# Kernel tuning notes

Hardware: AMD Instinct MI355X
Metric: run time of the kernel (lower is better)

Reference implementation:

```python
import jax, jax.numpy as jnp
import numpy as np

SOS = 4998
EOS = 4999
SCALING = 2.0


def setup_inputs() -> dict:
    key = jax.random.key(0)
    ks = jax.random.split(key, 12)
    B, T, E, D, A, C, F, ODIM, L = 32, 1000, 512, 1024, 512, 10, 100, 5000, 100
    s = 0.02
    return {
        "hpad": jax.random.normal(ks[0], (B, T, E), jnp.float32),
        "ys": jax.random.randint(ks[1], (B, L), 0, SOS, jnp.int32),
        # AttLoc params
        "w_enc": jax.random.normal(ks[2], (A, E), jnp.float32) * s,
        "b_enc": jnp.zeros((A,), jnp.float32),
        "w_dec": jax.random.normal(ks[3], (A, D), jnp.float32) * s,
        "w_att": jax.random.normal(ks[4], (A, C), jnp.float32) * s,
        "w_conv": jax.random.normal(ks[5], (C, 1, 2 * F + 1), jnp.float32) * s,  # OIH 1D conv kernel
        "w_gvec": jax.random.normal(ks[6], (1, A), jnp.float32) * s,
        "b_gvec": jnp.zeros((1,), jnp.float32),
        # Decoder params
        "embed": jax.random.normal(ks[7], (ODIM, D), jnp.float32) * s,
        "w_ih": jax.random.normal(ks[8], (4 * D, D + E), jnp.float32) * s,
        "w_hh": jax.random.normal(ks[9], (4 * D, D), jnp.float32) * s,
        "b_ih": jnp.zeros((4 * D,), jnp.float32),
        "b_hh": jnp.zeros((4 * D,), jnp.float32),
        "w_out": jax.random.normal(ks[10], (ODIM, D), jnp.float32) * s,
        "b_out": jnp.zeros((ODIM,), jnp.float32),
    }


def _decode(hpad, ys, w_enc, b_enc, w_dec, w_att, w_conv, w_gvec, b_gvec,
            embed, w_ih, w_hh, b_ih, b_hh, w_out, b_out):
    B, T, E = hpad.shape
    D = w_hh.shape[1]
    F = (w_conv.shape[-1] - 1) // 2
    # ys_in = [sos; y] per utterance (all same length -> already padded)
    ys_in = jnp.concatenate([jnp.full((B, 1), SOS, ys.dtype), ys], axis=1)  # [B, olen]
    eys = embed[ys_in]                                                      # [B, olen, D]
    # pre_compute_enc_h = mlp_enc(enc_h)
    pre = jnp.einsum('bte,ae->bta', hpad, w_enc) + b_enc                    # [B, T, A]
    att0 = jnp.full((B, T), 1.0 / T, hpad.dtype)   # uniform init attention (all hlen == T)
    z0 = jnp.zeros((B, D), hpad.dtype)
    c0 = jnp.zeros((B, D), hpad.dtype)

    def step(carry, ey_i):
        z, c, aw = carry
        # location-aware conv over previous attention weights: [B,1,T] -> [B,C,T]
        conv = jax.lax.conv_general_dilated(aw[:, None, :], w_conv, (1,), [(F, F)],
                                            dimension_numbers=('NCH', 'OIH', 'NCH'))
        att_feat = jnp.einsum('bct,ac->bta', conv, w_att)                   # mlp_att
        dec = (z @ w_dec.T)[:, None, :]                                     # mlp_dec, tiled
        e = jnp.tanh(att_feat + pre + dec) @ w_gvec[0] + b_gvec[0]          # [B, T]
        w = jax.nn.softmax(SCALING * e, axis=1)
        ctx = jnp.einsum('bt,bte->be', w, hpad)                             # [B, E]
        # LSTMCell
        x = jnp.concatenate([ey_i, ctx], axis=1)                            # [B, D+E]
        gates = x @ w_ih.T + b_ih + z @ w_hh.T + b_hh
        i_g, f_g, g_g, o_g = jnp.split(gates, 4, axis=1)
        c_new = jax.nn.sigmoid(f_g) * c + jax.nn.sigmoid(i_g) * jnp.tanh(g_g)
        z_new = jax.nn.sigmoid(o_g) * jnp.tanh(c_new)
        return (z_new, c_new, w), z_new

    _, z_all = jax.lax.scan(step, (z0, c0, att0), jnp.swapaxes(eys, 0, 1))  # [olen, B, D]
    y_all = jnp.einsum('obd,vd->obv', z_all, w_out) + b_out                 # [olen, B, odim]
    return jnp.swapaxes(y_all, 0, 1)                                        # [B, olen, odim]


def reference(hpad, ys, w_enc, b_enc, w_dec, w_att, w_conv, w_gvec, b_gvec,
              embed, w_ih, w_hh, b_ih, b_hh, w_out, b_out):
    return _decode(hpad, ys, w_enc, b_enc, w_dec, w_att, w_conv, w_gvec, b_gvec,
                   embed, w_ih, w_hh, b_ih, b_hh, w_out, b_out)
```

## Files before the change

kernel.cpp:

```cpp
#include <hip/hip_runtime.h>
#include <math.h>

#define B_    32
#define T_    1000
#define E_    512
#define D_    1024
#define A_    512
#define C_    10
#define F_    100
#define ODIM_ 5000
#define OLEN_ 101
#define SOS_  4998

#define OFF_PRE   0u
#define N_PRE     (32u*1000u*512u)
#define OFF_DEC   (OFF_PRE + N_PRE)
#define N_DEC     (32u*512u)
#define OFF_CONV  (OFF_DEC + N_DEC)
#define N_CONVB   (32u*10u*1000u)
#define OFF_EB    (OFF_CONV + N_CONVB)
#define N_EB      (32u*1000u)
#define OFF_AW    (OFF_EB + N_EB)
#define OFF_MS    (OFF_AW + N_EB)
#define N_MS      (32u*100u)
#define OFF_SS    (OFF_MS + N_MS)
#define OFF_CTX   (OFF_SS + N_MS)
#define N_CTX     (32u*512u)
#define OFF_GP    (OFF_CTX + N_CTX)
#define N_GP      (8u*32u*4096u)
#define OFF_Z     (OFF_GP + N_GP)
#define N_Z       (32u*1024u)
#define OFF_C     (OFF_Z + N_Z)
#define OFF_ZALL  (OFF_C + N_Z)

__device__ __forceinline__ float fast_tanh(float x) {
    float cx = fminf(8.f, fmaxf(-8.f, x));
    float e = __expf(2.f * cx);
    return (e - 1.f) * __builtin_amdgcn_rcpf(e + 1.f);
}
__device__ __forceinline__ float fast_sigmoid(float x) {
    float cx = fminf(30.f, fmaxf(-30.f, x));
    return __builtin_amdgcn_rcpf(1.f + __expf(-cx));
}

__global__ __launch_bounds__(256) void k_init(float* ws) {
    int i = blockIdx.x * 256 + threadIdx.x;
    if (i < (int)N_Z) { ws[OFF_Z + i] = 0.f; ws[OFF_C + i] = 0.f; }
    if (i < (int)N_CTX) ws[OFF_CTX + i] = 0.f;
    if (i < (int)N_EB) ws[OFF_AW + i] = 1.0f / (float)T_;
}

__global__ __launch_bounds__(256) void k_pre(const float* __restrict__ hp,
                                             const float* __restrict__ we,
                                             const float* __restrict__ be,
                                             float* __restrict__ pre) {
    __shared__ float As[64][68];
    __shared__ float Bs[64][68];
    int m0 = blockIdx.y * 64, n0 = blockIdx.x * 64;
    int tid = threadIdx.x;
    int tr = tid >> 4, tc = tid & 15;
    float acc[4][4] = {};
    for (int k0 = 0; k0 < 512; k0 += 64) {
        for (int i = tid; i < 1024; i += 256) {
            int m = i >> 4, kq = (i & 15) << 2;
            float4 v = *(const float4*)&hp[(size_t)(m0 + m) * 512 + k0 + kq];
            As[kq + 0][m] = v.x; As[kq + 1][m] = v.y; As[kq + 2][m] = v.z; As[kq + 3][m] = v.w;
            float4 w = *(const float4*)&we[(size_t)(n0 + m) * 512 + k0 + kq];
            Bs[kq + 0][m] = w.x; Bs[kq + 1][m] = w.y; Bs[kq + 2][m] = w.z; Bs[kq + 3][m] = w.w;
        }
        __syncthreads();
        #pragma unroll 16
        for (int kk = 0; kk < 64; ++kk) {
            float4 av = *(const float4*)&As[kk][tr << 2];
            float4 bv = *(const float4*)&Bs[kk][tc << 2];
            float a[4] = {av.x, av.y, av.z, av.w};
            float b[4] = {bv.x, bv.y, bv.z, bv.w};
            #pragma unroll
            for (int i = 0; i < 4; i++)
                #pragma unroll
                for (int j = 0; j < 4; j++) acc[i][j] += a[i] * b[j];
        }
        __syncthreads();
    }
    #pragma unroll
    for (int i = 0; i < 4; i++) {
        int m = m0 + (tr << 2) + i;
        int n = n0 + (tc << 2);
        float4 o;
        o.x = acc[i][0] + be[n + 0];
        o.y = acc[i][1] + be[n + 1];
        o.z = acc[i][2] + be[n + 2];
        o.w = acc[i][3] + be[n + 3];
        *(float4*)&pre[(size_t)m * 512 + n] = o;
    }
}

__global__ __launch_bounds__(256) void k_prepA(const float* __restrict__ wdec,
                                               const float* __restrict__ wconv,
                                               const float* __restrict__ wih,
                                               const float* __restrict__ whh,
                                               const float* __restrict__ embed,
                                               const int* __restrict__ ys,
                                               float* ws, int step) {
    int tid = threadIdx.x;
    if (blockIdx.x < 1024) {
        if (blockIdx.x < 64) ws[OFF_CTX + blockIdx.x * 256 + tid] = 0.f;
        int w = blockIdx.x * 4 + (tid >> 6);
        int lane = tid & 63;
        int a = w >> 3, bg = w & 7;
        const float4* wr = (const float4*)(wdec + (size_t)a * 1024);
        float4 w4[4];
        #pragma unroll
        for (int i = 0; i < 4; i++) w4[i] = wr[i * 64 + lane];
        float acc0 = 0.f, acc1 = 0.f, acc2 = 0.f, acc3 = 0.f;
        {
            const float4* zr = (const float4*)(ws + OFF_Z + (bg * 4 + 0) * 1024);
            #pragma unroll
            for (int i = 0; i < 4; i++) { float4 z4 = zr[i * 64 + lane];
                acc0 += w4[i].x*z4.x + w4[i].y*z4.y + w4[i].z*z4.z + w4[i].w*z4.w; }
        }
        {
            const float4* zr = (const float4*)(ws + OFF_Z + (bg * 4 + 1) * 1024);
            #pragma unroll
            for (int i = 0; i < 4; i++) { float4 z4 = zr[i * 64 + lane];
                acc1 += w4[i].x*z4.x + w4[i].y*z4.y + w4[i].z*z4.z + w4[i].w*z4.w; }
        }
        {
            const float4* zr = (const float4*)(ws + OFF_Z + (bg * 4 + 2) * 1024);
            #pragma unroll
            for (int i = 0; i < 4; i++) { float4 z4 = zr[i * 64 + lane];
                acc2 += w4[i].x*z4.x + w4[i].y*z4.y + w4[i].z*z4.z + w4[i].w*z4.w; }
        }
        {
            const float4* zr = (const float4*)(ws + OFF_Z + (bg * 4 + 3) * 1024);
            #pragma unroll
            for (int i = 0; i < 4; i++) { float4 z4 = zr[i * 64 + lane];
                acc3 += w4[i].x*z4.x + w4[i].y*z4.y + w4[i].z*z4.z + w4[i].w*z4.w; }
        }
        #pragma unroll
        for (int off = 32; off > 0; off >>= 1) {
            acc0 += __shfl_xor(acc0, off, 64);
            acc1 += __shfl_xor(acc1, off, 64);
            acc2 += __shfl_xor(acc2, off, 64);
            acc3 += __shfl_xor(acc3, off, 64);
        }
        if (lane == 0) {
            ws[OFF_DEC + (bg * 4 + 0) * 512 + a] = acc0;
            ws[OFF_DEC + (bg * 4 + 1) * 512 + a] = acc1;
            ws[OFF_DEC + (bg * 4 + 2) * 512 + a] = acc2;
            ws[OFF_DEC + (bg * 4 + 3) * 512 + a] = acc3;
        }
    } else if (blockIdx.x < 1344) {
        int blk = blockIdx.x - 1024;
        int b = blk / 10, c = blk - b * 10;
        if (tid >= 250) return;
        int t = tid * 4;
        const float* ar = ws + OFF_AW + b * 1000;
        const float* wc = wconv + c * 201;
        float a0, a1, a2, a3;
        a0 = (t - 100 >= 0) ? ar[t - 100] : 0.f;
        a1 = (t -  99 >= 0) ? ar[t -  99] : 0.f;
        a2 = (t -  98 >= 0) ? ar[t -  98] : 0.f;
        a3 = (t -  97 >= 0) ? ar[t -  97] : 0.f;
        float c0 = 0.f, c1 = 0.f, c2 = 0.f, c3 = 0.f;
        #pragma unroll 4
        for (int j = 0; j < 201; ++j) {
            float w = wc[j];
            c0 += a0 * w; c1 += a1 * w; c2 += a2 * w; c3 += a3 * w;
            a0 = a1; a1 = a2; a2 = a3;
            int ni = t + j - 96;
            a3 = (ni >= 0 && ni < 1000) ? ar[ni] : 0.f;
        }
        float* o = ws + OFF_CONV + (size_t)(b * 10 + c) * 1000 + t;
        o[0] = c0; o[1] = c1; o[2] = c2; o[3] = c3;
    } else {
        __shared__ float wlds[32][132];
        __shared__ float xs[32][36];
        int blk = blockIdx.x - 1344;
        int nt = blk & 31, ks = blk >> 5;
        int n0 = nt * 128;
        bool isE = (ks < 4);
        int kloc = isE ? ks * 256 : (ks - 4) * 256;
        int r = tid >> 1, h = tid & 1;
        int bx = tid >> 3, q8 = tid & 7;
        int tok = (step == 0) ? SOS_ : ys[bx * 100 + step - 1];
        const float* xsrc = isE ? (embed + (size_t)tok * 1024 + kloc)
                                : (ws + OFF_Z + (size_t)bx * 1024 + kloc);
        int nq = tid & 31, bq = tid >> 5;
        float acc[4][4] = {};
        for (int kc = 0; kc < 8; ++kc) {
            int koff = kc * 32;
            {
                const float* wrow = isE ? (wih + (size_t)(n0 + r) * 1536 + kloc + koff + h * 16)
                                        : (whh + (size_t)(n0 + r) * 1024 + kloc + koff + h * 16);
                #pragma unroll
                for (int j = 0; j < 4; ++j) {
                    float4 v = *(const float4*)&wrow[j * 4];
                    int kb = h * 16 + j * 4;
                    wlds[kb + 0][r] = v.x; wlds[kb + 1][r] = v.y;
                    wlds[kb + 2][r] = v.z; wlds[kb + 3][r] = v.w;
                }
            }
            {
                float4 v = *(const float4*)&xsrc[koff + q8 * 4];
                xs[q8 * 4 + 0][bx] = v.x; xs[q8 * 4 + 1][bx] = v.y;
                xs[q8 * 4 + 2][bx] = v.z; xs[q8 * 4 + 3][bx] = v.w;
            }
            __syncthreads();
            #pragma unroll 8
            for (int kk = 0; kk < 32; ++kk) {
                float4 wv = *(const float4*)&wlds[kk][nq * 4];
                float4 xv = *(const float4*)&xs[kk][bq * 4];
                float wa[4] = {wv.x, wv.y, wv.z, wv.w};
                float xa[4] = {xv.x, xv.y, xv.z, xv.w};
                #pragma unroll
                for (int i = 0; i < 4; i++)
                    #pragma unroll
                    for (int j = 0; j < 4; j++) acc[i][j] += wa[i] * xa[j];
            }
            __syncthreads();
        }
        float* gp = ws + OFF_GP + (size_t)(ks * 32 + bq * 4) * 4096 + n0 + nq * 4;
        #pragma unroll
        for (int j = 0; j < 4; j++)
            #pragma unroll
            for (int i = 0; i < 4; i++)
                gp[(size_t)j * 4096 + i] = acc[i][j];
    }
}

__global__ __launch_bounds__(256) void k_energy2(const float* __restrict__ watt,
                                                 const float* __restrict__ gvec,
                                                 const float* __restrict__ bg,
                                                 float* ws) {
    int w = blockIdx.x * 4 + (threadIdx.x >> 6);
    int lane = threadIdx.x & 63;
    int b = w / 100;
    int ch = w - b * 100;
    int t0 = ch * 10;
    int a0 = lane * 4, a1 = 256 + lane * 4;
    float wr[8][10];
    #pragma unroll
    for (int i = 0; i < 4; i++)
        #pragma unroll
        for (int c = 0; c < 10; c++) {
            wr[i][c]     = watt[(a0 + i) * 10 + c];
            wr[4 + i][c] = watt[(a1 + i) * 10 + c];
        }
    float4 d0 = *(const float4*)&ws[OFF_DEC + b * 512 + a0];
    float4 d1 = *(const float4*)&ws[OFF_DEC + b * 512 + a1];
    float4 g0 = *(const float4*)&gvec[a0];
    float4 g1 = *(const float4*)&gvec[a1];
    float dc[8] = {d0.x, d0.y, d0.z, d0.w, d1.x, d1.y, d1.z, d1.w};
    float gv[8] = {g0.x, g0.y, g0.z, g0.w, g1.x, g1.y, g1.z, g1.w};
    float bgv = bg[0];
    const float* convb = ws + OFF_CONV + b * 10000;
    float M = -1e30f, S = 0.f;
    for (int it = 0; it < 10; ++it) {
        int t = t0 + it;
        const float* pr = ws + OFF_PRE + (size_t)(b * 1000 + t) * 512;
        float4 p0 = *(const float4*)&pr[a0];
        float4 p1 = *(const float4*)&pr[a1];
        float cv[10];
        #pragma unroll
        for (int c = 0; c < 10; c++) cv[c] = convb[c * 1000 + t];
        float pa[8] = {p0.x, p0.y, p0.z, p0.w, p1.x, p1.y, p1.z, p1.w};
        float acc = 0.f;
        #pragma unroll
        for (int i = 0; i < 8; i++) {
            float s = pa[i] + dc[i];
            #pragma unroll
            for (int c = 0; c < 10; c++) s += cv[c] * wr[i][c];
            acc += gv[i] * fast_tanh(s);
        }
        #pragma unroll
        for (int off = 32; off > 0; off >>= 1) acc += __shfl_xor(acc, off, 64);
        float st = 2.f * (acc + bgv);
        if (lane == 0) ws[OFF_EB + b * 1000 + t] = st;
        float Mn = fmaxf(M, st);
        S = S * __expf(M - Mn) + __expf(st - Mn);
        M = Mn;
    }
    if (lane == 0) {
        ws[OFF_MS + b * 100 + ch] = M;
        ws[OFF_SS + b * 100 + ch] = S;
    }
}

__global__ __launch_bounds__(128) void k_ctx2(const float* __restrict__ hp, float* ws) {
    __shared__ float sm[100], ssum[100], wsh[32];
    int b = blockIdx.x >> 5, ts = blockIdx.x & 31;
    int tid = threadIdx.x;
    if (tid < 100) {
        sm[tid]   = ws[OFF_MS + b * 100 + tid];
        ssum[tid] = ws[OFF_SS + b * 100 + tid];
    }
    __syncthreads();
    float M = -1e30f;
    for (int i = 0; i < 100; i++) M = fmaxf(M, sm[i]);
    float S = 0.f;
    for (int i = 0; i < 100; i++) S += ssum[i] * __expf(sm[i] - M);
    float invS = __builtin_amdgcn_rcpf(S);
    int t0 = ts * 32;
    if (tid < 32) {
        int t = t0 + tid;
        float wv = 0.f;
        if (t < 1000) {
            wv = __expf(ws[OFF_EB + b * 1000 + t] - M) * invS;
            ws[OFF_AW + b * 1000 + t] = wv;
        }
        wsh[tid] = wv;
    }
    __syncthreads();
    int t1 = t0 + 32; if (t1 > 1000) t1 = 1000;
    const float4* hp4 = (const float4*)hp;
    float4 acc = make_float4(0.f, 0.f, 0.f, 0.f);
    for (int t = t0; t < t1; ++t) {
        float wv = wsh[t - t0];
        float4 h = hp4[(size_t)(b * 1000 + t) * 128 + tid];
        acc.x += wv * h.x; acc.y += wv * h.y; acc.z += wv * h.z; acc.w += wv * h.w;
    }
    float* cx = ws + OFF_CTX + b * 512 + tid * 4;
    atomicAdd(cx + 0, acc.x); atomicAdd(cx + 1, acc.y);
    atomicAdd(cx + 2, acc.z); atomicAdd(cx + 3, acc.w);
}

__global__ __launch_bounds__(128) void k_gl(const float* __restrict__ wih,
                                            const float* __restrict__ bih,
                                            const float* __restrict__ bhh,
                                            float* ws, int step) {
    __shared__ float wlds[32][36];
    __shared__ float xs[32][36];
    __shared__ float gl[32][33];
    int tid = threadIdx.x;
    int d0 = blockIdx.x * 8;
    int r = tid >> 2, h = tid & 3;
    int ng_r = (r >> 3) * 1024 + d0 + (r & 7);
    const float* wrow = wih + (size_t)ng_r * 1536 + 1024 + h * 8;
    int bx = tid >> 2, q4 = tid & 3;
    const float* xsrc = ws + OFF_CTX + (size_t)bx * 512 + q4 * 8;
    int nq = tid & 7, bq = tid >> 3;
    float acc[4][2] = {};
    for (int kc = 0; kc < 16; ++kc) {
        int k0 = kc * 32;
        {
            #pragma unroll
            for (int j = 0; j < 2; ++j) {
                float4 v = *(const float4*)&wrow[k0 + j * 4];
                int kb = h * 8 + j * 4;
                wlds[kb + 0][r] = v.x; wlds[kb + 1][r] = v.y;
                wlds[kb + 2][r] = v.z; wlds[kb + 3][r] = v.w;
            }
        }
        {
            #pragma unroll
            for (int j = 0; j < 2; ++j) {
                float4 v = *(const float4*)&xsrc[k0 + j * 4];
                int kb = q4 * 8 + j * 4;
                xs[kb + 0][bx] = v.x; xs[kb + 1][bx] = v.y;
                xs[kb + 2][bx] = v.z; xs[kb + 3][bx] = v.w;
            }
        }
        __syncthreads();
        #pragma unroll 8
        for (int kk = 0; kk < 32; ++kk) {
            float4 wv = *(const float4*)&wlds[kk][nq * 4];
            float x0 = xs[kk][bq * 2 + 0];
            float x1 = xs[kk][bq * 2 + 1];
            acc[0][0] += wv.x * x0; acc[0][1] += wv.x * x1;
            acc[1][0] += wv.y * x0; acc[1][1] += wv.y * x1;
            acc[2][0] += wv.z * x0; acc[2][1] += wv.z * x1;
            acc[3][0] += wv.w * x0; acc[3][1] += wv.w * x1;
        }
        __syncthreads();
    }
    #pragma unroll
    for (int i = 0; i < 4; i++) {
        int nl = nq * 4 + i;
        int ng = (nl >> 3) * 1024 + d0 + (nl & 7);
        float bb = bih[ng] + bhh[ng];
        #pragma unroll
        for (int j = 0; j < 2; j++) {
            int b = bq * 2 + j;
            float s = acc[i][j] + bb;
            #pragma unroll
            for (int sl = 0; sl < 8; sl++)
                s += ws[OFF_GP + (size_t)(sl * 32 + b) * 4096 + ng];
            gl[nl][b] = s;
        }
    }
    __syncthreads();
    #pragma unroll
    for (int u = 0; u < 2; u++) {
        int o = tid * 2 + u;
        int dl = o >> 5, b = o & 31;
        float gi = gl[dl][b];
        float gf = gl[8 + dl][b];
        float gg = gl[16 + dl][b];
        float go = gl[24 + dl][b];
        int id = b * 1024 + d0 + dl;
        float c_old = ws[OFF_C + id];
        float si = fast_sigmoid(gi);
        float sf = fast_sigmoid(gf);
        float so = fast_sigmoid(go);
        float cn = sf * c_old + si * fast_tanh(gg);
        float hh = so * fast_tanh(cn);
        ws[OFF_C + id] = cn;
        ws[OFF_Z + id] = hh;
        ws[OFF_ZALL + ((size_t)step * 32 + b) * 1024 + d0 + dl] = hh;
    }
}

__global__ __launch_bounds__(256) void k_out(const float* __restrict__ zall,
                                             const float* __restrict__ wo,
                                             const float* __restrict__ bo,
                                             float* __restrict__ out) {
    __shared__ float As[64][68];
    __shared__ float Bs[64][68];
    int m0 = blockIdx.y * 64, n0 = blockIdx.x * 64;
    int tid = threadIdx.x;
    int tr = tid >> 4, tc = tid & 15;
    float acc[4][4] = {};
    for (int k0 = 0; k0 < 1024; k0 += 64) {
        for (int i = tid; i < 1024; i += 256) {
            int m = i >> 4, kq = (i & 15) << 2;
            int gm = m0 + m;
            float4 v = (gm < 3232) ? *(const float4*)&zall[(size_t)gm * 1024 + k0 + kq]
                                   : make_float4(0.f, 0.f, 0.f, 0.f);
            As[kq + 0][m] = v.x; As[kq + 1][m] = v.y; As[kq + 2][m] = v.z; As[kq + 3][m] = v.w;
            int gn = n0 + m;
            float4 w = (gn < 5000) ? *(const float4*)&wo[(size_t)gn * 1024 + k0 + kq]
                                   : make_float4(0.f, 0.f, 0.f, 0.f);
            Bs[kq + 0][m] = w.x; Bs[kq + 1][m] = w.y; Bs[kq + 2][m] = w.z; Bs[kq + 3][m] = w.w;
        }
        __syncthreads();
        #pragma unroll 16
        for (int kk = 0; kk < 64; ++kk) {
            float4 av = *(const float4*)&As[kk][tr << 2];
            float4 bv = *(const float4*)&Bs[kk][tc << 2];
            float a[4] = {av.x, av.y, av.z, av.w};
            float b[4] = {bv.x, bv.y, bv.z, bv.w};
            #pragma unroll
            for (int i = 0; i < 4; i++)
                #pragma unroll
                for (int j = 0; j < 4; j++) acc[i][j] += a[i] * b[j];
        }
        __syncthreads();
    }
    #pragma unroll
    for (int i = 0; i < 4; i++) {
        int m = m0 + (tr << 2) + i;
        if (m >= 3232) continue;
        int b = m & 31, o = m >> 5;
        #pragma unroll
        for (int j = 0; j < 4; j++) {
            int v = n0 + (tc << 2) + j;
            if (v < 5000)
                out[((size_t)b * 101 + o) * 5000 + v] = acc[i][j] + bo[v];
        }
    }
}

extern "C" void kernel_launch(void* const* d_in, const int* in_sizes, int n_in,
                              void* d_out, int out_size, void* d_ws, size_t ws_size,
                              hipStream_t stream) {
    const float* hpad   = (const float*)d_in[0];
    const int*   ys     = (const int*)d_in[1];
    const float* w_enc  = (const float*)d_in[2];
    const float* b_enc  = (const float*)d_in[3];
    const float* w_dec  = (const float*)d_in[4];
    const float* w_att  = (const float*)d_in[5];
    const float* w_conv = (const float*)d_in[6];
    const float* w_gvec = (const float*)d_in[7];
    const float* b_gvec = (const float*)d_in[8];
    const float* embed  = (const float*)d_in[9];
    const float* w_ih   = (const float*)d_in[10];
    const float* w_hh   = (const float*)d_in[11];
    const float* b_ih   = (const float*)d_in[12];
    const float* b_hh   = (const float*)d_in[13];
    const float* w_out  = (const float*)d_in[14];
    const float* b_out  = (const float*)d_in[15];
    float* ws  = (float*)d_ws;
    float* out = (float*)d_out;

    k_init<<<128, 256, 0, stream>>>(ws);
    k_pre<<<dim3(8, 500), 256, 0, stream>>>(hpad, w_enc, b_enc, ws + OFF_PRE);

    for (int step = 0; step < OLEN_; ++step) {
        k_prepA<<<1600, 256, 0, stream>>>(w_dec, w_conv, w_ih, w_hh, embed, ys, ws, step);
        k_energy2<<<800, 256, 0, stream>>>(w_att, w_gvec, b_gvec, ws);
        k_ctx2<<<1024, 128, 0, stream>>>(hpad, ws);
        k_gl<<<128, 128, 0, stream>>>(w_ih, b_ih, b_hh, ws, step);
    }

    k_out<<<dim3(79, 51), 256, 0, stream>>>(ws + OFF_ZALL, w_out, b_out, out);
}
```

Baseline: 11.00 ms.

## Fuse per-step decoder kernels into one persistent cooperative kernel with grid syncs

Replaces the four per-step kernel launches (404 total) with a single cooperative persistent kernel of 512 blocks that runs all decoder steps, separated by grid-wide syncs, and keeps a multi-launch fallback. It also transposes the precomputed encoder projection to [B,A,T] so the energy phase reads contiguous time values. It defers softmax normalisation by storing unnormalised exponentials, accumulating row sums atomically and scaling later in the conv and context/gate phases. Intended to remove launch overhead and separate max/sum passes, at the cost of grid-sync latency, lower parallelism per phase and dropping the max-subtraction for numerical stability.

```diff
diff --git a/kernel.cpp b/kernel.cpp
--- a/kernel.cpp
+++ b/kernel.cpp
@@ -1,5 +1,8 @@
 #include <hip/hip_runtime.h>
+#include <hip/hip_cooperative_groups.h>
 #include <math.h>
+
+namespace cg = cooperative_groups;
 
 #define B_    32
 #define T_    1000
@@ -13,18 +16,16 @@
 #define SOS_  4998
 
 #define OFF_PRE   0u
-#define N_PRE     (32u*1000u*512u)
+#define N_PRE     (32u*512u*1000u)
 #define OFF_DEC   (OFF_PRE + N_PRE)
 #define N_DEC     (32u*512u)
 #define OFF_CONV  (OFF_DEC + N_DEC)
 #define N_CONVB   (32u*10u*1000u)
-#define OFF_EB    (OFF_CONV + N_CONVB)
-#define N_EB      (32u*1000u)
-#define OFF_AW    (OFF_EB + N_EB)
-#define OFF_MS    (OFF_AW + N_EB)
-#define N_MS      (32u*100u)
-#define OFF_SS    (OFF_MS + N_MS)
-#define OFF_CTX   (OFF_SS + N_MS)
+#define OFF_AW    (OFF_CONV + N_CONVB)
+#define N_AW      (32u*1000u)
+#define OFF_S     (OFF_AW + N_AW)
+#define N_S       (64u)
+#define OFF_CTX   (OFF_S + N_S)
 #define N_CTX     (32u*512u)
 #define OFF_GP    (OFF_CTX + N_CTX)
 #define N_GP      (8u*32u*4096u)
@@ -47,23 +48,29 @@
     int i = blockIdx.x * 256 + threadIdx.x;
     if (i < (int)N_Z) { ws[OFF_Z + i] = 0.f; ws[OFF_C + i] = 0.f; }
     if (i < (int)N_CTX) ws[OFF_CTX + i] = 0.f;
-    if (i < (int)N_EB) ws[OFF_AW + i] = 1.0f / (float)T_;
-}
-
-__global__ __launch_bounds__(256) void k_pre(const float* __restrict__ hp,
-                                             const float* __restrict__ we,
-                                             const float* __restrict__ be,
-                                             float* __restrict__ pre) {
+    if (i < (int)N_AW) ws[OFF_AW + i] = 1.0f;
+    if (i < 64) ws[OFF_S + i] = (i >= 32) ? 1000.f : 0.f;
+}
+
+__global__ __launch_bounds__(256) void k_pre_t(const float* __restrict__ hp,
+                                               const float* __restrict__ we,
+                                               const float* __restrict__ be,
+                                               float* __restrict__ pre_t) {
     __shared__ float As[64][68];
     __shared__ float Bs[64][68];
-    int m0 = blockIdx.y * 64, n0 = blockIdx.x * 64;
+    int bt = blockIdx.y;
+    int b = bt >> 4, tc = bt & 15;
+    int t0 = tc * 64;
+    int n0 = blockIdx.x * 64;
     int tid = threadIdx.x;
-    int tr = tid >> 4, tc = tid & 15;
+    int tr = tid >> 4, tcl = tid & 15;
     float acc[4][4] = {};
     for (int k0 = 0; k0 < 512; k0 += 64) {
         for (int i = tid; i < 1024; i += 256) {
             int m = i >> 4, kq = (i & 15) << 2;
-            float4 v = *(const float4*)&hp[(size_t)(m0 + m) * 512 + k0 + kq];
+            int t = t0 + m;
+            float4 v = (t < 1000) ? *(const float4*)&hp[((size_t)(b * 1000 + t)) * 512 + k0 + kq]
+                                  : make_float4(0.f, 0.f, 0.f, 0.f);
             As[kq + 0][m] = v.x; As[kq + 1][m] = v.y; As[kq + 2][m] = v.z; As[kq + 3][m] = v.w;
             float4 w = *(const float4*)&we[(size_t)(n0 + m) * 512 + k0 + kq];
             Bs[kq + 0][m] = w.x; Bs[kq + 1][m] = w.y; Bs[kq + 2][m] = w.z; Bs[kq + 3][m] = w.w;
@@ -72,88 +79,70 @@
         #pragma unroll 16
         for (int kk = 0; kk < 64; ++kk) {
             float4 av = *(const float4*)&As[kk][tr << 2];
-            float4 bv = *(const float4*)&Bs[kk][tc << 2];
+            float4 bv = *(const float4*)&Bs[kk][tcl << 2];
             float a[4] = {av.x, av.y, av.z, av.w};
-            float b[4] = {bv.x, bv.y, bv.z, bv.w};
+            float bq[4] = {bv.x, bv.y, bv.z, bv.w};
             #pragma unroll
             for (int i = 0; i < 4; i++)
                 #pragma unroll
-                for (int j = 0; j < 4; j++) acc[i][j] += a[i] * b[j];
-        }
-        __syncthreads();
-    }
+                for (int j = 0; j < 4; j++) acc[i][j] += a[i] * bq[j];
+        }
+        __syncthreads();
+    }
+    int tt = t0 + (tr << 2);
+    if (tt < 1000) {
+        #pragma unroll
+        for (int j = 0; j < 4; ++j) {
+            int a = n0 + (tcl << 2) + j;
+            float bea = be[a];
+            float4 o = make_float4(acc[0][j] + bea, acc[1][j] + bea,
+                                   acc[2][j] + bea, acc[3][j] + bea);
+            *(float4*)&pre_t[((size_t)(b * 512 + a)) * 1000 + tt] = o;
+        }
+    }
+}
+
+
+__device__ __forceinline__ void dec_unit(int u, int tid, const float* __restrict__ wdec,
+                                         float* ws, int step) {
+    if (u < 64) ws[OFF_CTX + u * 256 + tid] = 0.f;
+    if (u == 64 && tid < 32) ws[OFF_S + (step & 1) * 32 + tid] = 0.f;
+    int w = u * 4 + (tid >> 6);
+    int lane = tid & 63;
+    int a = w >> 3, bg7 = w & 7;
+    const float4* wr = (const float4*)(wdec + (size_t)a * 1024);
+    float4 w4[4];
     #pragma unroll
-    for (int i = 0; i < 4; i++) {
-        int m = m0 + (tr << 2) + i;
-        int n = n0 + (tc << 2);
-        float4 o;
-        o.x = acc[i][0] + be[n + 0];
-        o.y = acc[i][1] + be[n + 1];
-        o.z = acc[i][2] + be[n + 2];
-        o.w = acc[i][3] + be[n + 3];
-        *(float4*)&pre[(size_t)m * 512 + n] = o;
-    }
-}
-
-__global__ __launch_bounds__(256) void k_prepA(const float* __restrict__ wdec,
-                                               const float* __restrict__ wconv,
-                                               const float* __restrict__ wih,
-                                               const float* __restrict__ whh,
-                                               const float* __restrict__ embed,
-                                               const int* __restrict__ ys,
-                                               float* ws, int step) {
-    int tid = threadIdx.x;
-    if (blockIdx.x < 1024) {
-        if (blockIdx.x < 64) ws[OFF_CTX + blockIdx.x * 256 + tid] = 0.f;
-        int w = blockIdx.x * 4 + (tid >> 6);
-        int lane = tid & 63;
-        int a = w >> 3, bg = w & 7;
-        const float4* wr = (const float4*)(wdec + (size_t)a * 1024);
-        float4 w4[4];
-        #pragma unroll
-        for (int i = 0; i < 4; i++) w4[i] = wr[i * 64 + lane];
-        float acc0 = 0.f, acc1 = 0.f, acc2 = 0.f, acc3 = 0.f;
-        {
-            const float4* zr = (const float4*)(ws + OFF_Z + (bg * 4 + 0) * 1024);
-            #pragma unroll
-            for (int i = 0; i < 4; i++) { float4 z4 = zr[i * 64 + lane];
-                acc0 += w4[i].x*z4.x + w4[i].y*z4.y + w4[i].z*z4.z + w4[i].w*z4.w; }
-        }
-        {
-            const float4* zr = (const float4*)(ws + OFF_Z + (bg * 4 + 1) * 1024);
-            #pragma unroll
-            for (int i = 0; i < 4; i++) { float4 z4 = zr[i * 64 + lane];
-                acc1 += w4[i].x*z4.x + w4[i].y*z4.y + w4[i].z*z4.z + w4[i].w*z4.w; }
-        }
-        {
-            const float4* zr = (const float4*)(ws + OFF_Z + (bg * 4 + 2) * 1024);
-            #pragma unroll
-            for (int i = 0; i < 4; i++) { float4 z4 = zr[i * 64 + lane];
-                acc2 += w4[i].x*z4.x + w4[i].y*z4.y + w4[i].z*z4.z + w4[i].w*z4.w; }
-        }
-        {
-            const float4* zr = (const float4*)(ws + OFF_Z + (bg * 4 + 3) * 1024);
-            #pragma unroll
-            for (int i = 0; i < 4; i++) { float4 z4 = zr[i * 64 + lane];
-                acc3 += w4[i].x*z4.x + w4[i].y*z4.y + w4[i].z*z4.z + w4[i].w*z4.w; }
-        }
-        #pragma unroll
-        for (int off = 32; off > 0; off >>= 1) {
-            acc0 += __shfl_xor(acc0, off, 64);
-            acc1 += __shfl_xor(acc1, off, 64);
-            acc2 += __shfl_xor(acc2, off, 64);
-            acc3 += __shfl_xor(acc3, off, 64);
-        }
-        if (lane == 0) {
-            ws[OFF_DEC + (bg * 4 + 0) * 512 + a] = acc0;
-            ws[OFF_DEC + (bg * 4 + 1) * 512 + a] = acc1;
-            ws[OFF_DEC + (bg * 4 + 2) * 512 + a] = acc2;
-            ws[OFF_DEC + (bg * 4 + 3) * 512 + a] = acc3;
-        }
-    } else if (blockIdx.x < 1344) {
-        int blk = blockIdx.x - 1024;
-        int b = blk / 10, c = blk - b * 10;
-        if (tid >= 250) return;
+    for (int i = 0; i < 4; i++) w4[i] = wr[i * 64 + lane];
+    float acc[4] = {0.f, 0.f, 0.f, 0.f};
+    #pragma unroll
+    for (int bb = 0; bb < 4; ++bb) {
+        const float4* zr = (const float4*)(ws + OFF_Z + (size_t)(bg7 * 4 + bb) * 1024);
+        #pragma unroll
+        for (int i = 0; i < 4; i++) {
+            float4 z4 = zr[i * 64 + lane];
+            acc[bb] += w4[i].x * z4.x + w4[i].y * z4.y + w4[i].z * z4.z + w4[i].w * z4.w;
+        }
+    }
+    #pragma unroll
+    for (int off = 32; off > 0; off >>= 1) {
+        acc[0] += __shfl_xor(acc[0], off, 64);
+        acc[1] += __shfl_xor(acc[1], off, 64);
+        acc[2] += __shfl_xor(acc[2], off, 64);
+        acc[3] += __shfl_xor(acc[3], off, 64);
+    }
+    if (lane == 0) {
+        #pragma unroll
+        for (int bb = 0; bb < 4; ++bb)
+            ws[OFF_DEC + (bg7 * 4 + bb) * 512 + a] = acc[bb];
+    }
+}
+
+__device__ __forceinline__ void conv_unit(int u2, int tid, const float* __restrict__ wconv,
+                                          float* ws, int step) {
+    int b = u2 / 10, c = u2 - b * 10;
+    if (tid < 250) {
+        float invS = __builtin_amdgcn_rcpf(ws[OFF_S + ((step + 1) & 1) * 32 + b]);
         int t = tid * 4;
         const float* ar = ws + OFF_AW + b * 1000;
         const float* wc = wconv + c * 201;
@@ -172,243 +161,289 @@
             a3 = (ni >= 0 && ni < 1000) ? ar[ni] : 0.f;
         }
         float* o = ws + OFF_CONV + (size_t)(b * 10 + c) * 1000 + t;
-        o[0] = c0; o[1] = c1; o[2] = c2; o[3] = c3;
-    } else {
-        __shared__ float wlds[32][132];
-        __shared__ float xs[32][36];
-        int blk = blockIdx.x - 1344;
-        int nt = blk & 31, ks = blk >> 5;
-        int n0 = nt * 128;
-        bool isE = (ks < 4);
-        int kloc = isE ? ks * 256 : (ks - 4) * 256;
-        int r = tid >> 1, h = tid & 1;
+        o[0] = c0 * invS; o[1] = c1 * invS; o[2] = c2 * invS; o[3] = c3 * invS;
+    }
+}
+
+__device__ __forceinline__ void gates_unit(int u3, int tid, float* smem,
+                                           const float* __restrict__ wih,
+                                           const float* __restrict__ whh,
+                                           const float* __restrict__ embed,
+                                           const int* __restrict__ ys,
+                                           float* ws, int step) {
+    float* wlds = smem;
+    float* xs   = smem + 4224;
+    int nt = u3 & 31, ks = u3 >> 5;
+    int n0 = nt * 128;
+    bool isE = (ks < 4);
+    int kloc = isE ? ks * 256 : (ks - 4) * 256;
+    int r = tid >> 1, h = tid & 1;
+    int bx = tid >> 3, q8 = tid & 7;
+    int tok = (step == 0) ? SOS_ : ys[bx * 100 + step - 1];
+    const float* xsrc = isE ? (embed + (size_t)tok * 1024 + kloc)
+                            : (ws + OFF_Z + (size_t)bx * 1024 + kloc);
+    int nq = tid & 31, bq = tid >> 5;
+    float acc[4][4] = {};
+    for (int kc = 0; kc < 8; ++kc) {
+        int koff = kc * 32;
+        {
+            const float* wrow = isE ? (wih + (size_t)(n0 + r) * 1536 + kloc + koff + h * 16)
+                                    : (whh + (size_t)(n0 + r) * 1024 + kloc + koff + h * 16);
+            #pragma unroll
+            for (int j = 0; j < 4; ++j) {
+                float4 v = *(const float4*)&wrow[j * 4];
+                int kb = h * 16 + j * 4;
+                wlds[(kb + 0) * 132 + r] = v.x; wlds[(kb + 1) * 132 + r] = v.y;
+                wlds[(kb + 2) * 132 + r] = v.z; wlds[(kb + 3) * 132 + r] = v.w;
+            }
+        }
+        {
+            float4 v = *(const float4*)&xsrc[koff + q8 * 4];
+            xs[(q8 * 4 + 0) * 36 + bx] = v.x; xs[(q8 * 4 + 1) * 36 + bx] = v.y;
+            xs[(q8 * 4 + 2) * 36 + bx] = v.z; xs[(q8 * 4 + 3) * 36 + bx] = v.w;
+        }
+        __syncthreads();
+        #pragma unroll 8
+        for (int kk = 0; kk < 32; ++kk) {
+            float4 wv = *(const float4*)&wlds[kk * 132 + nq * 4];
+            float4 xv = *(const float4*)&xs[kk * 36 + bq * 4];
+            float wa[4] = {wv.x, wv.y, wv.z, wv.w};
+            float xa[4] = {xv.x, xv.y, xv.z, xv.w};
+            #pragma unroll
+            for (int i = 0; i < 4; i++)
+                #pragma unroll
+                for (int j = 0; j < 4; j++) acc[i][j] += wa[i] * xa[j];
+        }
+        __syncthreads();
+    }
+    float* gp = ws + OFF_GP + (size_t)(ks * 32 + bq * 4) * 4096 + n0 + nq * 4;
+    #pragma unroll
+    for (int j = 0; j < 4; j++)
+        #pragma unroll
+        for (int i = 0; i < 4; i++)
+            gp[(size_t)j * 4096 + i] = acc[i][j];
+}
+
+__device__ __forceinline__ void phase1(int bid, int tid, float* smem,
+                                       const float* wdec, const float* wconv,
+                                       const float* wih, const float* whh,
+                                       const float* embed, const int* ys,
+                                       float* ws, int step) {
+    for (int u = bid; u < 1600; u += 512) {
+        if (u < 1024)       dec_unit(u, tid, wdec, ws, step);
+        else if (u < 1344)  conv_unit(u - 1024, tid, wconv, ws, step);
+        else                gates_unit(u - 1344, tid, smem, wih, whh, embed, ys, ws, step);
+    }
+}
+
+__device__ __forceinline__ void phase2(int bid, int tid, float* smem,
+                                       const float* __restrict__ watt,
+                                       const float* __restrict__ gvec,
+                                       const float* __restrict__ bgv,
+                                       float* ws, int step) {
+    if (bid < 256) {
+        int b = bid >> 3, tc = bid & 7;
+        int tbase = tc * 128;
+        int w = tid >> 6, l = tid & 63;
+        int t = tbase + l * 2;
+        bool valid = (t < 1000);
+        float2 cvv[10];
+        const float* convb = ws + OFF_CONV + b * 10000;
+        #pragma unroll
+        for (int c = 0; c < 10; ++c)
+            cvv[c] = valid ? *(const float2*)&convb[c * 1000 + t] : make_float2(0.f, 0.f);
+        const float* decb = ws + OFF_DEC + b * 512;
+        int a0 = w * 128;
+        const float* pt = ws + OFF_PRE + ((size_t)(b * 512 + a0)) * 1000 + t;
+        float ex = 0.f, ey = 0.f;
+        #pragma unroll 2
+        for (int a = a0; a < a0 + 128; ++a) {
+            float2 p2 = valid ? *(const float2*)pt : make_float2(0.f, 0.f);
+            pt += 1000;
+            float da = decb[a];
+            float sx = p2.x + da, sy = p2.y + da;
+            const float* wa = watt + a * 10;
+            #pragma unroll
+            for (int c = 0; c < 10; ++c) {
+                float wv = wa[c];
+                sx += cvv[c].x * wv; sy += cvv[c].y * wv;
+            }
+            float gva = gvec[a];
+            ex += gva * fast_tanh(sx);
+            ey += gva * fast_tanh(sy);
+        }
+        float* part = smem;
+        part[w * 128 + l * 2]     = ex;
+        part[w * 128 + l * 2 + 1] = ey;
+        __syncthreads();
+        float wtil = 0.f;
+        if (tid < 128) {
+            int tt = tbase + tid;
+            float e = part[tid] + part[128 + tid] + part[256 + tid] + part[384 + tid];
+            if (tt < 1000) {
+                wtil = __expf(2.f * (e + bgv[0]));
+                ws[OFF_AW + b * 1000 + tt] = wtil;
+            }
+        }
+        __syncthreads();
+        part[tid] = wtil;
+        __syncthreads();
+        for (int off = 128; off >= 1; off >>= 1) {
+            if (tid < off) part[tid] += part[tid + off];
+            __syncthreads();
+        }
+        if (tid == 0) atomicAdd(&ws[OFF_S + (step & 1) * 32 + b], part[0]);
+    }
+}
+
+__device__ __forceinline__ void phase3(int bid, int tid, float* smem,
+                                       const float* __restrict__ hp, float* ws) {
+    int b = bid >> 4, ts = bid & 15;
+    int t0 = ts * 64;
+    float* wsh = smem;
+    if (tid < 64) {
+        int t = t0 + tid;
+        wsh[tid] = (t < 1000) ? ws[OFF_AW + b * 1000 + t] : 0.f;
+    }
+    __syncthreads();
+    int e4 = tid & 127, th = tid >> 7;
+    const float4* hp4 = (const float4*)hp;
+    float4 acc = make_float4(0.f, 0.f, 0.f, 0.f);
+    int tstart = t0 + th * 32;
+    int tend = tstart + 32; if (tend > 1000) tend = 1000;
+    for (int t = tstart; t < tend; ++t) {
+        float wv = wsh[t - t0];
+        float4 h = hp4[((size_t)(b * 1000 + t)) * 128 + e4];
+        acc.x += wv * h.x; acc.y += wv * h.y; acc.z += wv * h.z; acc.w += wv * h.w;
+    }
+    float* cx = ws + OFF_CTX + b * 512 + e4 * 4;
+    atomicAdd(cx + 0, acc.x); atomicAdd(cx + 1, acc.y);
+    atomicAdd(cx + 2, acc.z); atomicAdd(cx + 3, acc.w);
+    __syncthreads();
+}
+
+__device__ __forceinline__ void phase4(int bid, int tid, float* smem,
+                                       const float* __restrict__ wih,
+                                       const float* __restrict__ bih,
+                                       const float* __restrict__ bhh,
+                                       float* ws, int step) {
+    if (bid < 128) {
+        float* wlds = smem;
+        float* xs   = smem + 1152;
+        float* glb  = smem + 2304;
+        float* sinv = smem + 3360;
+        int d0 = bid * 8;
+        if (tid < 32) sinv[tid] = __builtin_amdgcn_rcpf(ws[OFF_S + (step & 1) * 32 + tid]);
+        __syncthreads();
+        int r = tid >> 3, h = tid & 7;
+        int ng_r = (r >> 3) * 1024 + d0 + (r & 7);
+        const float* wrow = wih + (size_t)ng_r * 1536 + 1024 + h * 4;
         int bx = tid >> 3, q8 = tid & 7;
-        int tok = (step == 0) ? SOS_ : ys[bx * 100 + step - 1];
-        const float* xsrc = isE ? (embed + (size_t)tok * 1024 + kloc)
-                                : (ws + OFF_Z + (size_t)bx * 1024 + kloc);
-        int nq = tid & 31, bq = tid >> 5;
-        float acc[4][4] = {};
-        for (int kc = 0; kc < 8; ++kc) {
-            int koff = kc * 32;
+        const float* xsrc = ws + OFF_CTX + (size_t)bx * 512 + q8 * 4;
+        float xscale = sinv[bx];
+        int nq = tid & 15, bq = tid >> 4;
+        float acc[2][2] = {};
+        for (int kc = 0; kc < 16; ++kc) {
+            int k0 = kc * 32;
             {
-                const float* wrow = isE ? (wih + (size_t)(n0 + r) * 1536 + kloc + koff + h * 16)
-                                        : (whh + (size_t)(n0 + r) * 1024 + kloc + koff + h * 16);
-                #pragma unroll
-                for (int j = 0; j < 4; ++j) {
-                    float4 v = *(const float4*)&wrow[j * 4];
-                    int kb = h * 16 + j * 4;
-                    wlds[kb + 0][r] = v.x; wlds[kb + 1][r] = v.y;
-                    wlds[kb + 2][r] = v.z; wlds[kb + 3][r] = v.w;
-                }
+                float4 v = *(const float4*)&wrow[k0];
+                wlds[(h * 4 + 0) * 36 + r] = v.x; wlds[(h * 4 + 1) * 36 + r] = v.y;
+                wlds[(h * 4 + 2) * 36 + r] = v.z; wlds[(h * 4 + 3) * 36 + r] = v.w;
             }
             {
-                float4 v = *(const float4*)&xsrc[koff + q8 * 4];
-                xs[q8 * 4 + 0][bx] = v.x; xs[q8 * 4 + 1][bx] = v.y;
-                xs[q8 * 4 + 2][bx] = v.z; xs[q8 * 4 + 3][bx] = v.w;
+                float4 v = *(const float4*)&xsrc[k0];
+                xs[(q8 * 4 + 0) * 36 + bx] = v.x * xscale; xs[(q8 * 4 + 1) * 36 + bx] = v.y * xscale;
+                xs[(q8 * 4 + 2) * 36 + bx] = v.z * xscale; xs[(q8 * 4 + 3) * 36 + bx] = v.w * xscale;
             }
             __syncthreads();
             #pragma unroll 8
             for (int kk = 0; kk < 32; ++kk) {
-                float4 wv = *(const float4*)&wlds[kk][nq * 4];
-                float4 xv = *(const float4*)&xs[kk][bq * 4];
-                float wa[4] = {wv.x, wv.y, wv.z, wv.w};
-                float xa[4] = {xv.x, xv.y, xv.z, xv.w};
-                #pragma unroll
-                for (int i = 0; i < 4; i++)
-                    #pragma unroll
-                    for (int j = 0; j < 4; j++) acc[i][j] += wa[i] * xa[j];
+                float w0 = wlds[kk * 36 + nq * 2], w1 = wlds[kk * 36 + nq * 2 + 1];
+                float x0 = xs[kk * 36 + bq * 2],  x1 = xs[kk * 36 + bq * 2 + 1];
+                acc[0][0] += w0 * x0; acc[0][1] += w0 * x1;
+                acc[1][0] += w1 * x0; acc[1][1] += w1 * x1;
             }
             __syncthreads();
         }
-        float* gp = ws + OFF_GP + (size_t)(ks * 32 + bq * 4) * 4096 + n0 + nq * 4;
-        #pragma unroll
-        for (int j = 0; j < 4; j++)
-            #pragma unroll
-            for (int i = 0; i < 4; i++)
-                gp[(size_t)j * 4096 + i] = acc[i][j];
-    }
-}
-
-__global__ __launch_bounds__(256) void k_energy2(const float* __restrict__ watt,
-                                                 const float* __restrict__ gvec,
-                                                 const float* __restrict__ bg,
-                                                 float* ws) {
-    int w = blockIdx.x * 4 + (threadIdx.x >> 6);
-    int lane = threadIdx.x & 63;
-    int b = w / 100;
-    int ch = w - b * 100;
-    int t0 = ch * 10;
-    int a0 = lane * 4, a1 = 256 + lane * 4;
-    float wr[8][10];
-    #pragma unroll
-    for (int i = 0; i < 4; i++)
-        #pragma unroll
-        for (int c = 0; c < 10; c++) {
-            wr[i][c]     = watt[(a0 + i) * 10 + c];
-            wr[4 + i][c] = watt[(a1 + i) * 10 + c];
-        }
-    float4 d0 = *(const float4*)&ws[OFF_DEC + b * 512 + a0];
-    float4 d1 = *(const float4*)&ws[OFF_DEC + b * 512 + a1];
-    float4 g0 = *(const float4*)&gvec[a0];
-    float4 g1 = *(const float4*)&gvec[a1];
-    float dc[8] = {d0.x, d0.y, d0.z, d0.w, d1.x, d1.y, d1.z, d1.w};
-    float gv[8] = {g0.x, g0.y, g0.z, g0.w, g1.x, g1.y, g1.z, g1.w};
-    float bgv = bg[0];
-    const float* convb = ws + OFF_CONV + b * 10000;
-    float M = -1e30f, S = 0.f;
-    for (int it = 0; it < 10; ++it) {
-        int t = t0 + it;
-        const float* pr = ws + OFF_PRE + (size_t)(b * 1000 + t) * 512;
-        float4 p0 = *(const float4*)&pr[a0];
-        float4 p1 = *(const float4*)&pr[a1];
-        float cv[10];
-        #pragma unroll
-        for (int c = 0; c < 10; c++) cv[c] = convb[c * 1000 + t];
-        float pa[8] = {p0.x, p0.y, p0.z, p0.w, p1.x, p1.y, p1.z, p1.w};
-        float acc = 0.f;
-        #pragma unroll
-        for (int i = 0; i < 8; i++) {
-            float s = pa[i] + dc[i];
-            #pragma unroll
-            for (int c = 0; c < 10; c++) s += cv[c] * wr[i][c];
-            acc += gv[i] * fast_tanh(s);
-        }
-        #pragma unroll
-        for (int off = 32; off > 0; off >>= 1) acc += __shfl_xor(acc, off, 64);
-        float st = 2.f * (acc + bgv);
-        if (lane == 0) ws[OFF_EB + b * 1000 + t] = st;
-        float Mn = fmaxf(M, st);
-        S = S * __expf(M - Mn) + __expf(st - Mn);
-        M = Mn;
-    }
-    if (lane == 0) {
-        ws[OFF_MS + b * 100 + ch] = M;
-        ws[OFF_SS + b * 100 + ch] = S;
-    }
-}
-
-__global__ __launch_bounds__(128) void k_ctx2(const float* __restrict__ hp, float* ws) {
-    __shared__ float sm[100], ssum[100], wsh[32];
-    int b = blockIdx.x >> 5, ts = blockIdx.x & 31;
-    int tid = threadIdx.x;
-    if (tid < 100) {
-        sm[tid]   = ws[OFF_MS + b * 100 + tid];
-        ssum[tid] = ws[OFF_SS + b * 100 + tid];
-    }
-    __syncthreads();
-    float M = -1e30f;
-    for (int i = 0; i < 100; i++) M = fmaxf(M, sm[i]);
-    float S = 0.f;
-    for (int i = 0; i < 100; i++) S += ssum[i] * __expf(sm[i] - M);
-    float invS = __builtin_amdgcn_rcpf(S);
-    int t0 = ts * 32;
-    if (tid < 32) {
-        int t = t0 + tid;
-        float wv = 0.f;
-        if (t < 1000) {
-            wv = __expf(ws[OFF_EB + b * 1000 + t] - M) * invS;
-            ws[OFF_AW + b * 1000 + t] = wv;
-        }
-        wsh[tid] = wv;
-    }
-    __syncthreads();
-    int t1 = t0 + 32; if (t1 > 1000) t1 = 1000;
-    const float4* hp4 = (const float4*)hp;
-    float4 acc = make_float4(0.f, 0.f, 0.f, 0.f);
-    for (int t = t0; t < t1; ++t) {
-        float wv = wsh[t - t0];
-        float4 h = hp4[(size_t)(b * 1000 + t) * 128 + tid];
-        acc.x += wv * h.x; acc.y += wv * h.y; acc.z += wv * h.z; acc.w += wv * h.w;
-    }
-    float* cx = ws + OFF_CTX + b * 512 + tid * 4;
-    atomicAdd(cx + 0, acc.x); atomicAdd(cx + 1, acc.y);
-    atomicAdd(cx + 2, acc.z); atomicAdd(cx + 3, acc.w);
-}
-
-__global__ __launch_bounds__(128) void k_gl(const float* __restrict__ wih,
-                                            const float* __restrict__ bih,
-                                            const float* __restrict__ bhh,
-                                            float* ws, int step) {
-    __shared__ float wlds[32][36];
-    __shared__ float xs[32][36];
-    __shared__ float gl[32][33];
-    int tid = threadIdx.x;
-    int d0 = blockIdx.x * 8;
-    int r = tid >> 2, h = tid & 3;
-    int ng_r = (r >> 3) * 1024 + d0 + (r & 7);
-    const float* wrow = wih + (size_t)ng_r * 1536 + 1024 + h * 8;
-    int bx = tid >> 2, q4 = tid & 3;
-    const float* xsrc = ws + OFF_CTX + (size_t)bx * 512 + q4 * 8;
-    int nq = tid & 7, bq = tid >> 3;
-    float acc[4][2] = {};
-    for (int kc = 0; kc < 16; ++kc) {
-        int k0 = kc * 32;
-        {
+        #pragma unroll
+        for (int i = 0; i < 2; ++i) {
+            int nl = nq * 2 + i;
+            int ng = (nl >> 3) * 1024 + d0 + (nl & 7);
+            float bb = bih[ng] + bhh[ng];
             #pragma unroll
             for (int j = 0; j < 2; ++j) {
-                float4 v = *(const float4*)&wrow[k0 + j * 4];
-                int kb = h * 8 + j * 4;
-                wlds[kb + 0][r] = v.x; wlds[kb + 1][r] = v.y;
-                wlds[kb + 2][r] = v.z; wlds[kb + 3][r] = v.w;
-            }
-        }
+                int b = bq * 2 + j;
+                float s = acc[i][j] + bb;
+                #pragma unroll
+                for (int sl = 0; sl < 8; ++sl)
+                    s += ws[OFF_GP + (size_t)(sl * 32 + b) * 4096 + ng];
+                glb[nl * 33 + b] = s;
+            }
+        }
+        __syncthreads();
         {
-            #pragma unroll
-            for (int j = 0; j < 2; ++j) {
-                float4 v = *(const float4*)&xsrc[k0 + j * 4];
-                int kb = q4 * 8 + j * 4;
-                xs[kb + 0][bx] = v.x; xs[kb + 1][bx] = v.y;
-                xs[kb + 2][bx] = v.z; xs[kb + 3][bx] = v.w;
-            }
-        }
-        __syncthreads();
-        #pragma unroll 8
-        for (int kk = 0; kk < 32; ++kk) {
-            float4 wv = *(const float4*)&wlds[kk][nq * 4];
-            float x0 = xs[kk][bq * 2 + 0];
-            float x1 = xs[kk][bq * 2 + 1];
-            acc[0][0] += wv.x * x0; acc[0][1] += wv.x * x1;
-            acc[1][0] += wv.y * x0; acc[1][1] += wv.y * x1;
-            acc[2][0] += wv.z * x0; acc[2][1] += wv.z * x1;
-            acc[3][0] += wv.w * x0; acc[3][1] += wv.w * x1;
-        }
-        __syncthreads();
-    }
-    #pragma unroll
-    for (int i = 0; i < 4; i++) {
-        int nl = nq * 4 + i;
-        int ng = (nl >> 3) * 1024 + d0 + (nl & 7);
-        float bb = bih[ng] + bhh[ng];
-        #pragma unroll
-        for (int j = 0; j < 2; j++) {
-            int b = bq * 2 + j;
-            float s = acc[i][j] + bb;
-            #pragma unroll
-            for (int sl = 0; sl < 8; sl++)
-                s += ws[OFF_GP + (size_t)(sl * 32 + b) * 4096 + ng];
-            gl[nl][b] = s;
-        }
-    }
-    __syncthreads();
-    #pragma unroll
-    for (int u = 0; u < 2; u++) {
-        int o = tid * 2 + u;
-        int dl = o >> 5, b = o & 31;
-        float gi = gl[dl][b];
-        float gf = gl[8 + dl][b];
-        float gg = gl[16 + dl][b];
-        float go = gl[24 + dl][b];
-        int id = b * 1024 + d0 + dl;
-        float c_old = ws[OFF_C + id];
-        float si = fast_sigmoid(gi);
-        float sf = fast_sigmoid(gf);
-        float so = fast_sigmoid(go);
-        float cn = sf * c_old + si * fast_tanh(gg);
-        float hh = so * fast_tanh(cn);
-        ws[OFF_C + id] = cn;
-        ws[OFF_Z + id] = hh;
-        ws[OFF_ZALL + ((size_t)step * 32 + b) * 1024 + d0 + dl] = hh;
-    }
+            int dl = tid >> 5, b = tid & 31;
+            float gi = glb[dl * 33 + b];
+            float gf = glb[(8 + dl) * 33 + b];
+            float gg = glb[(16 + dl) * 33 + b];
+            float go = glb[(24 + dl) * 33 + b];
+            int id = b * 1024 + d0 + dl;
+            float c_old = ws[OFF_C + id];
+            float si = fast_sigmoid(gi);
+            float sf = fast_sigmoid(gf);
+            float so = fast_sigmoid(go);
+            float cn = sf * c_old + si * fast_tanh(gg);
+            float hh = so * fast_tanh(cn);
+            ws[OFF_C + id] = cn;
+            ws[OFF_Z + id] = hh;
+            ws[OFF_ZALL + ((size_t)step * 32 + b) * 1024 + d0 + dl] = hh;
+        }
+        __syncthreads();
+    }
+}
+
+__global__ __launch_bounds__(256, 2) void k_loop(const float* hpad, const int* ys,
+                                                 const float* wdec, const float* wconv,
+                                                 const float* watt, const float* gvec,
+                                                 const float* bgv, const float* embed,
+                                                 const float* wih, const float* whh,
+                                                 const float* bih, const float* bhh,
+                                                 float* ws) {
+    cg::grid_group grd = cg::this_grid();
+    __shared__ float smem[5376];
+    int bid = blockIdx.x, tid = threadIdx.x;
+    for (int step = 0; step < OLEN_; ++step) {
+        phase1(bid, tid, smem, wdec, wconv, wih, whh, embed, ys, ws, step);
+        grd.sync();
+        phase2(bid, tid, smem, watt, gvec, bgv, ws, step);
+        grd.sync();
+        phase3(bid, tid, smem, hpad, ws);
+        grd.sync();
+        phase4(bid, tid, smem, wih, bih, bhh, ws, step);
+        grd.sync();
+    }
+}
+
+__global__ __launch_bounds__(256, 2) void k_p1(const float* wdec, const float* wconv,
+                                               const float* wih, const float* whh,
+                                               const float* embed, const int* ys,
+                                               float* ws, int step) {
+    __shared__ float smem[5376];
+    phase1(blockIdx.x, threadIdx.x, smem, wdec, wconv, wih, whh, embed, ys, ws, step);
+}
+__global__ __launch_bounds__(256, 2) void k_p2(const float* watt, const float* gvec,
+                                               const float* bgv, float* ws, int step) {
+    __shared__ float smem[5376];
+    phase2(blockIdx.x, threadIdx.x, smem, watt, gvec, bgv, ws, step);
+}
+__global__ __launch_bounds__(256, 2) void k_p3(const float* hpad, float* ws) {
+    __shared__ float smem[5376];
+    phase3(blockIdx.x, threadIdx.x, smem, hpad, ws);
+}
+__global__ __launch_bounds__(256, 2) void k_p4(const float* wih, const float* bih,
+                                               const float* bhh, float* ws, int step) {
+    __shared__ float smem[5376];
+    phase4(blockIdx.x, threadIdx.x, smem, wih, bih, bhh, ws, step);
 }
 
 __global__ __launch_bounds__(256) void k_out(const float* __restrict__ zall,
@@ -484,13 +519,24 @@
     float* out = (float*)d_out;
 
     k_init<<<128, 256, 0, stream>>>(ws);
-    k_pre<<<dim3(8, 500), 256, 0, stream>>>(hpad, w_enc, b_enc, ws + OFF_PRE);
-
-    for (int step = 0; step < OLEN_; ++step) {
-        k_prepA<<<1600, 256, 0, stream>>>(w_dec, w_conv, w_ih, w_hh, embed, ys, ws, step);
-        k_energy2<<<800, 256, 0, stream>>>(w_att, w_gvec, b_gvec, ws);
-        k_ctx2<<<1024, 128, 0, stream>>>(hpad, ws);
-        k_gl<<<128, 128, 0, stream>>>(w_ih, b_ih, b_hh, ws, step);
+    k_pre_t<<<dim3(8, 512), 256, 0, stream>>>(hpad, w_enc, b_enc, ws + OFF_PRE);
+
+    void* kargs[13];
+    kargs[0]  = (void*)&hpad;  kargs[1]  = (void*)&ys;    kargs[2]  = (void*)&w_dec;
+    kargs[3]  = (void*)&w_conv; kargs[4] = (void*)&w_att; kargs[5]  = (void*)&w_gvec;
+    kargs[6]  = (void*)&b_gvec; kargs[7] = (void*)&embed; kargs[8]  = (void*)&w_ih;
+    kargs[9]  = (void*)&w_hh;  kargs[10] = (void*)&b_ih;  kargs[11] = (void*)&b_hh;
+    kargs[12] = (void*)&ws;
+    hipError_t cerr = hipLaunchCooperativeKernel(reinterpret_cast<void*>(k_loop),
+                                                 dim3(512), dim3(256), kargs, 0, stream);
+    if (cerr != hipSuccess) {
+        (void)hipGetLastError();
+        for (int step = 0; step < OLEN_; ++step) {
+            k_p1<<<512, 256, 0, stream>>>(w_dec, w_conv, w_ih, w_hh, embed, ys, ws, step);
+            k_p2<<<256, 256, 0, stream>>>(w_att, w_gvec, b_gvec, ws, step);
+            k_p3<<<512, 256, 0, stream>>>(hpad, ws);
+            k_p4<<<128, 256, 0, stream>>>(w_ih, b_ih, b_hh, ws, step);
+        }
     }
 
     k_out<<<dim3(79, 51), 256, 0, stream>>>(ws + OFF_ZALL, w_out, b_out, out);
```

After: 34.27 ms. 3.12x slower.
